# Performance work log

Measured on AMD Instinct MI355X. Metric: run time of the kernel, lower is better.

Reference implementation:

```python
import jax, jax.numpy as jnp
import numpy as np

N_NODES = 100000
N_EDGES = 3200000
D_FEAT = 256
FILTERS = 256


def setup_inputs() -> dict:
    key = jax.random.key(0)
    k1, k2, k3, k4, k5 = jax.random.split(key, 5)
    x = jax.random.normal(k1, (N_NODES, D_FEAT), dtype=jnp.float32)
    edge_row = jax.random.randint(k2, (N_EDGES,), 0, N_NODES, dtype=jnp.int32)
    edge_col = jax.random.randint(k3, (N_EDGES,), 0, N_NODES, dtype=jnp.int32)
    edge_vals = jnp.ones((N_EDGES,), dtype=jnp.float32)
    w = jax.random.normal(k4, (D_FEAT, FILTERS), dtype=jnp.float32) * (2.0 / D_FEAT) ** 0.5  # he_normal
    b = jax.random.normal(k5, (FILTERS,), dtype=jnp.float32) * 0.05
    return {"x": x, "edge_row": edge_row, "edge_col": edge_col,
            "edge_vals": edge_vals, "w": w, "b": b}


def reference(x, edge_row, edge_col, edge_vals, w, b):
    n = x.shape[0]
    # normalize_A: D = rowsum(A); L = D^{-1/2} A D^{-1/2}
    deg = jax.ops.segment_sum(edge_vals, edge_row, num_segments=n)
    dinv = jnp.where(deg > 0, deg ** -0.5, 0.0)  # [N]
    norm_vals = edge_vals * dinv[edge_row] * dinv[edge_col]  # [E]
    # dense projection then sparse aggregation + bias + relu
    h = x @ w  # [N, F]
    msg = norm_vals[:, None] * h[edge_col]  # [E, F] gather + scale
    agg = jax.ops.segment_sum(msg, edge_row, num_segments=n)  # [N, F]
    return jax.nn.relu(agg + b)
```

## Files before the change

### kernel.cpp

```cpp
#include <hip/hip_runtime.h>
#include <hip/hip_bf16.h>


#define DF   256
#define RSH  7
#define RPB  128
#define CAP  4800
#define CHUNK 8192

typedef __attribute__((ext_vector_type(8))) short short8;
typedef __attribute__((ext_vector_type(4))) float f32x4;

__device__ __forceinline__ unsigned short f2bf(float f) {
    unsigned int u = __float_as_uint(f);
    unsigned int r = (u + 0x7fffu + ((u >> 16) & 1u)) >> 16;
    return (unsigned short)r;
}
__device__ __forceinline__ unsigned int pack2(float a, float b) {
    return (unsigned)f2bf(a) | ((unsigned)f2bf(b) << 16);
}
__device__ __forceinline__ float bflo(unsigned int u) { return __uint_as_float(u << 16); }
__device__ __forceinline__ float bfhi(unsigned int u) { return __uint_as_float(u & 0xffff0000u); }

__global__ __launch_bounds__(256) void bhist_kernel(const int* __restrict__ row,
                                                    int* __restrict__ blockhist, int NB, int E) {
    __shared__ int hist[1024];
    int t = threadIdx.x;
    for (int i = t; i < NB; i += 256) hist[i] = 0;
    __syncthreads();
    int base = blockIdx.x * CHUNK;
    int end = base + CHUNK; if (end > E) end = E;
    for (int i = base + t; i < end; i += 256)
        atomicAdd(&hist[row[i] >> RSH], 1);
    __syncthreads();
    for (int i = t; i < NB; i += 256)
        blockhist[(size_t)blockIdx.x * NB + i] = hist[i];
}

__global__ __launch_bounds__(256) void bscan_kernel(int* __restrict__ blockhist,
                                                    int* __restrict__ buckettot, int NB, int NBLK) {
    __shared__ int ps[256];
    int b = blockIdx.x, t = threadIdx.x;
    int e0 = 2 * t, e1 = 2 * t + 1;
    int v0 = (e0 < NBLK) ? blockhist[(size_t)e0 * NB + b] : 0;
    int v1 = (e1 < NBLK) ? blockhist[(size_t)e1 * NB + b] : 0;
    int tsum = v0 + v1;
    ps[t] = tsum;
    __syncthreads();
    for (int off = 1; off < 256; off <<= 1) {
        int v = (t >= off) ? ps[t - off] : 0;
        __syncthreads();
        ps[t] += v;
        __syncthreads();
    }
    int pre = ps[t] - tsum;
    if (e0 < NBLK) blockhist[(size_t)e0 * NB + b] = pre;
    if (e1 < NBLK) blockhist[(size_t)e1 * NB + b] = pre + v0;
    if (t == 255) buckettot[b] = ps[255];
}

__global__ __launch_bounds__(1024) void btot_kernel(const int* __restrict__ buckettot,
                                                    int* __restrict__ bucket_base, int NB) {
    __shared__ int ps[1024];
    int t = threadIdx.x;
    int v = (t < NB) ? buckettot[t] : 0;
    ps[t] = v;
    __syncthreads();
    for (int off = 1; off < 1024; off <<= 1) {
        int u = (t >= off) ? ps[t - off] : 0;
        __syncthreads();
        ps[t] += u;
        __syncthreads();
    }
    if (t < NB) bucket_base[t] = ps[t] - v;
    if (t == 1023) bucket_base[NB] = ps[1023];
}

__global__ __launch_bounds__(256) void bscatter_kernel(const int* __restrict__ row,
                                                       const int* __restrict__ col,
                                                       const float* __restrict__ vals,
                                                       const int* __restrict__ blockhist,
                                                       const int* __restrict__ bucket_base,
                                                       int2* __restrict__ bedge, int NB, int E) {
    __shared__ int loff[1024];
    int t = threadIdx.x, blk = blockIdx.x;
    for (int i = t; i < NB; i += 256)
        loff[i] = bucket_base[i] + blockhist[(size_t)blk * NB + i];
    __syncthreads();
    int base = blk * CHUNK;
    int end = base + CHUNK; if (end > E) end = E;
    for (int i = base + t; i < end; i += 256) {
        int r = row[i];
        int p = atomicAdd(&loff[r >> RSH], 1);
        bedge[p] = make_int2(((r & (RPB - 1)) << 17) | col[i], __float_as_int(vals[i]));
    }
}

__global__ __launch_bounds__(256) void deg_kernel(const int2* __restrict__ bedge,
                                                  const int* __restrict__ bucket_base,
                                                  float* __restrict__ dinv, int N) {
    __shared__ float acc[RPB];
    int b = blockIdx.x, t = threadIdx.x;
    if (t < RPB) acc[t] = 0.f;
    __syncthreads();
    int s = bucket_base[b], e = bucket_base[b + 1];
    for (int i = s + t; i < e; i += 256) {
        int2 ed = bedge[i];
        atomicAdd(&acc[ed.x >> 17], __int_as_float(ed.y));
    }
    __syncthreads();
    if (t < RPB) {
        int r = b * RPB + t;
        if (r < N) {
            float d = acc[t];
            dinv[r] = (d > 0.f) ? (1.0f / sqrtf(d)) : 0.f;
        }
    }
}

__global__ __launch_bounds__(256) void transpose_kernel(const float* __restrict__ w,
                                                        float* __restrict__ wT) {
    __shared__ float tile[32][33];
    int bx = blockIdx.x * 32, by = blockIdx.y * 32;
    int tx = threadIdx.x, ty = threadIdx.y;
    for (int j = ty; j < 32; j += 8) tile[j][tx] = w[(by + j) * DF + bx + tx];
    __syncthreads();
    for (int j = ty; j < 32; j += 8) wT[(bx + j) * DF + by + tx] = tile[tx][j];
}

__global__ __launch_bounds__(256) void gemm_kernel(const float* __restrict__ x,
                                                   const float* __restrict__ wT,
                                                   const float* __restrict__ dinv,
                                                   unsigned short* __restrict__ h, int N) {
    __shared__ unsigned short Al[128 * 32];
    __shared__ unsigned short Bl[128 * 32];
    int tid = threadIdx.x;
    int by = blockIdx.x, bx = blockIdx.y;
    int wv = tid >> 6, lane = tid & 63;
    int wr = wv >> 1, wc = wv & 1;
    int q = lane >> 4, mi = lane & 15;

    f32x4 acc[4][4];
#pragma unroll
    for (int i = 0; i < 4; ++i)
#pragma unroll
        for (int j = 0; j < 4; ++j) acc[i][j] = (f32x4){0.f, 0.f, 0.f, 0.f};

    int srow = tid >> 1;
    int sseg = (tid & 1) * 16;
    int axrow = by * 128 + srow; if (axrow >= N) axrow = N - 1;
    const float* ax = x + (long)axrow * DF + sseg;
    const float* bxp = wT + (long)(bx * 128 + srow) * DF + sseg;
    unsigned short* Aw = &Al[srow * 32 + sseg];
    unsigned short* Bw = &Bl[srow * 32 + sseg];

    for (int kk = 0; kk < DF; kk += 32) {
        float4 a0 = *(const float4*)(ax + kk);
        float4 a1 = *(const float4*)(ax + kk + 4);
        float4 a2 = *(const float4*)(ax + kk + 8);
        float4 a3 = *(const float4*)(ax + kk + 12);
        float4 b0 = *(const float4*)(bxp + kk);
        float4 b1 = *(const float4*)(bxp + kk + 4);
        float4 b2 = *(const float4*)(bxp + kk + 8);
        float4 b3 = *(const float4*)(bxp + kk + 12);
        __syncthreads();
        uint4 pa, pb;
        pa.x = pack2(a0.x, a0.y); pa.y = pack2(a0.z, a0.w);
        pa.z = pack2(a1.x, a1.y); pa.w = pack2(a1.z, a1.w);
        *(uint4*)Aw = pa;
        pa.x = pack2(a2.x, a2.y); pa.y = pack2(a2.z, a2.w);
        pa.z = pack2(a3.x, a3.y); pa.w = pack2(a3.z, a3.w);
        *(uint4*)(Aw + 8) = pa;
        pb.x = pack2(b0.x, b0.y); pb.y = pack2(b0.z, b0.w);
        pb.z = pack2(b1.x, b1.y); pb.w = pack2(b1.z, b1.w);
        *(uint4*)Bw = pb;
        pb.x = pack2(b2.x, b2.y); pb.y = pack2(b2.z, b2.w);
        pb.z = pack2(b3.x, b3.y); pb.w = pack2(b3.z, b3.w);
        *(uint4*)(Bw + 8) = pb;
        __syncthreads();

        short8 af[4], bf[4];
#pragma unroll
        for (int i = 0; i < 4; ++i)
            af[i] = *(const short8*)&Al[(wr * 64 + i * 16 + mi) * 32 + q * 8];
#pragma unroll
        for (int j = 0; j < 4; ++j)
            bf[j] = *(const short8*)&Bl[(wc * 64 + j * 16 + mi) * 32 + q * 8];
#pragma unroll
        for (int i = 0; i < 4; ++i)
#pragma unroll
            for (int j = 0; j < 4; ++j)
                acc[i][j] = __builtin_amdgcn_mfma_f32_16x16x32_bf16(af[i], bf[j], acc[i][j], 0, 0, 0);
    }

#pragma unroll
    for (int i = 0; i < 4; ++i) {
        int base_row = by * 128 + wr * 64 + i * 16 + q * 4;
#pragma unroll
        for (int r = 0; r < 4; ++r) {
            int rg = base_row + r;
            if (rg < N) {
                float dv = dinv[rg];
#pragma unroll
                for (int j = 0; j < 4; ++j) {
                    int cg = bx * 128 + wc * 64 + j * 16 + mi;
                    h[(long)rg * DF + cg] = f2bf(dv * acc[i][j][r]);
                }
            }
        }
    }
}

__global__ __launch_bounds__(256) void aggb_kernel(const unsigned short* __restrict__ h,
                                                   const int2* __restrict__ bedge,
                                                   const int* __restrict__ bucket_base,
                                                   const float* __restrict__ dinv,
                                                   const float* __restrict__ bias,
                                                   float* __restrict__ out, int N) {
    __shared__ int2 ledge[CAP];
    __shared__ int cnt[RPB];
    __shared__ int lrs[RPB + 1];
    __shared__ int lfill[RPB];
    int b = blockIdx.x, t = threadIdx.x;
    int s = bucket_base[b], e = bucket_base[b + 1];
    int tot = e - s;
    int cap_end = s + (tot < CAP ? tot : CAP);
    if (t < RPB) { cnt[t] = 0; lfill[t] = 0; }
    __syncthreads();
    for (int i = s + t; i < cap_end; i += 256)
        atomicAdd(&cnt[bedge[i].x >> 17], 1);
    __syncthreads();
    int myc = 0;
    if (t < RPB) { myc = cnt[t]; lrs[t] = myc; }
    __syncthreads();
    for (int off = 1; off < RPB; off <<= 1) {
        int v = (t < RPB && t >= off) ? lrs[t - off] : 0;
        __syncthreads();
        if (t < RPB) lrs[t] += v;
        __syncthreads();
    }
    if (t < RPB) {
        int iv = lrs[t];
        lrs[t] = iv - myc;
        if (t == RPB - 1) lrs[RPB] = iv;
    }
    __syncthreads();
    for (int i = s + t; i < cap_end; i += 256) {
        int2 ed = bedge[i];
        int rl = ed.x >> 17;
        int p = lrs[rl] + atomicAdd(&lfill[rl], 1);
        ledge[p] = make_int2(ed.x & 0x1FFFF, ed.y);
    }
    __syncthreads();
    int wv = t >> 6, lane = t & 63;
    int half = lane >> 5;
    int fl = (lane & 31) * 8;
    const unsigned short* hp = h + fl;
    for (int lr = wv; lr < RPB; lr += 4) {
        int r = b * RPB + lr;
        if (r >= N) break;
        int rs = lrs[lr], re = lrs[lr + 1];
        float a0 = 0, a1 = 0, a2 = 0, a3 = 0, a4 = 0, a5 = 0, a6 = 0, a7 = 0;
        int i = rs + half;
        for (; i + 6 < re; i += 8) {
            int2 e0 = ledge[i], e1 = ledge[i + 2], e2 = ledge[i + 4], e3 = ledge[i + 6];
            uint4 u0 = *(const uint4*)(hp + (long)e0.x * DF);
            uint4 u1 = *(const uint4*)(hp + (long)e1.x * DF);
            uint4 u2 = *(const uint4*)(hp + (long)e2.x * DF);
            uint4 u3 = *(const uint4*)(hp + (long)e3.x * DF);
            float v0 = __int_as_float(e0.y), v1 = __int_as_float(e1.y);
            float v2 = __int_as_float(e2.y), v3 = __int_as_float(e3.y);
            a0 += v0 * bflo(u0.x) + v1 * bflo(u1.x) + v2 * bflo(u2.x) + v3 * bflo(u3.x);
            a1 += v0 * bfhi(u0.x) + v1 * bfhi(u1.x) + v2 * bfhi(u2.x) + v3 * bfhi(u3.x);
            a2 += v0 * bflo(u0.y) + v1 * bflo(u1.y) + v2 * bflo(u2.y) + v3 * bflo(u3.y);
            a3 += v0 * bfhi(u0.y) + v1 * bfhi(u1.y) + v2 * bfhi(u2.y) + v3 * bfhi(u3.y);
            a4 += v0 * bflo(u0.z) + v1 * bflo(u1.z) + v2 * bflo(u2.z) + v3 * bflo(u3.z);
            a5 += v0 * bfhi(u0.z) + v1 * bfhi(u1.z) + v2 * bfhi(u2.z) + v3 * bfhi(u3.z);
            a6 += v0 * bflo(u0.w) + v1 * bflo(u1.w) + v2 * bflo(u2.w) + v3 * bflo(u3.w);
            a7 += v0 * bfhi(u0.w) + v1 * bfhi(u1.w) + v2 * bfhi(u2.w) + v3 * bfhi(u3.w);
        }
        for (; i < re; i += 2) {
            int2 e0 = ledge[i];
            float v0 = __int_as_float(e0.y);
            uint4 u0 = *(const uint4*)(hp + (long)e0.x * DF);
            a0 += v0 * bflo(u0.x); a1 += v0 * bfhi(u0.x);
            a2 += v0 * bflo(u0.y); a3 += v0 * bfhi(u0.y);
            a4 += v0 * bflo(u0.z); a5 += v0 * bfhi(u0.z);
            a6 += v0 * bflo(u0.w); a7 += v0 * bfhi(u0.w);
        }
        for (int j = cap_end + half; j < e; j += 2) {
            int2 ed = bedge[j];
            if ((ed.x >> 17) == lr) {
                float v0 = __int_as_float(ed.y);
                uint4 u0 = *(const uint4*)(hp + (long)(ed.x & 0x1FFFF) * DF);
                a0 += v0 * bflo(u0.x); a1 += v0 * bfhi(u0.x);
                a2 += v0 * bflo(u0.y); a3 += v0 * bfhi(u0.y);
                a4 += v0 * bflo(u0.z); a5 += v0 * bfhi(u0.z);
                a6 += v0 * bflo(u0.w); a7 += v0 * bfhi(u0.w);
            }
        }
        a0 += __shfl_xor(a0, 32); a1 += __shfl_xor(a1, 32);
        a2 += __shfl_xor(a2, 32); a3 += __shfl_xor(a3, 32);
        a4 += __shfl_xor(a4, 32); a5 += __shfl_xor(a5, 32);
        a6 += __shfl_xor(a6, 32); a7 += __shfl_xor(a7, 32);
        if (half == 0) {
            float dr = dinv[r];
            float4 b0 = *(const float4*)(bias + fl);
            float4 b1 = *(const float4*)(bias + fl + 4);
            float4 o0, o1;
            o0.x = fmaxf(fmaf(dr, a0, b0.x), 0.f);
            o0.y = fmaxf(fmaf(dr, a1, b0.y), 0.f);
            o0.z = fmaxf(fmaf(dr, a2, b0.z), 0.f);
            o0.w = fmaxf(fmaf(dr, a3, b0.w), 0.f);
            o1.x = fmaxf(fmaf(dr, a4, b1.x), 0.f);
            o1.y = fmaxf(fmaf(dr, a5, b1.y), 0.f);
            o1.z = fmaxf(fmaf(dr, a6, b1.z), 0.f);
            o1.w = fmaxf(fmaf(dr, a7, b1.w), 0.f);
            *(float4*)(out + (long)r * DF + fl) = o0;
            *(float4*)(out + (long)r * DF + fl + 4) = o1;
        }
    }
}

extern "C" void kernel_launch(void* const* d_in, const int* in_sizes, int n_in,
                              void* d_out, int out_size, void* d_ws, size_t ws_size,
                              hipStream_t stream) {
    const float* x   = (const float*)d_in[0];
    const int* erow  = (const int*)d_in[1];
    const int* ecol  = (const int*)d_in[2];
    const float* ev  = (const float*)d_in[3];
    const float* w   = (const float*)d_in[4];
    const float* b   = (const float*)d_in[5];
    float* out = (float*)d_out;

    int N = in_sizes[0] / DF;
    int E = in_sizes[1];
    int NB = (N + RPB - 1) >> RSH;
    int NBLK = (E + CHUNK - 1) / CHUNK;

    char* ws = (char*)d_ws;
    size_t Ea8 = (((size_t)E * 8) + 255) & ~(size_t)255;
    size_t Hs  = (((size_t)N * DF * 2) + 255) & ~(size_t)255;
    size_t Na  = (((size_t)N * 4) + 255) & ~(size_t)255;

    int2* bedge = (int2*)ws;
    char* reg2 = ws + Ea8;
    unsigned short* h = (unsigned short*)reg2;
    int* blockhist = (int*)reg2;
    char* reg3 = reg2 + Hs;
    float* wT = (float*)reg3;
    float* dinv = (float*)(reg3 + 262144);
    int* buckettot = (int*)(reg3 + 262144 + Na);
    int* bucket_base = (int*)(reg3 + 262144 + Na + 8192);

    bhist_kernel<<<NBLK, 256, 0, stream>>>(erow, blockhist, NB, E);
    bscan_kernel<<<NB, 256, 0, stream>>>(blockhist, buckettot, NB, NBLK);
    btot_kernel<<<1, 1024, 0, stream>>>(buckettot, bucket_base, NB);
    bscatter_kernel<<<NBLK, 256, 0, stream>>>(erow, ecol, ev, blockhist, bucket_base, bedge, NB, E);
    deg_kernel<<<NB, 256, 0, stream>>>(bedge, bucket_base, dinv, N);
    transpose_kernel<<<dim3(8, 8), dim3(32, 8), 0, stream>>>(w, wT);
    gemm_kernel<<<dim3((N + 127) / 128, DF / 128), 256, 0, stream>>>(x, wT, dinv, h, N);
    aggb_kernel<<<NB, 256, 0, stream>>>(h, bedge, bucket_base, dinv, b, out, N);
}
```

Measured before the change: 595.9 us.

## Build full CSR in degree pass; one-wave-per-row aggregation; full-width bf16 GEMM

The degree kernel now also does the per-bucket counting sort and writes a global CSR (row starts plus sorted col/val pairs). Aggregation then drops the LDS staging, the CAP overflow path and the per-block scans, and runs one wave per row across many small blocks for better occupancy and load balance. The GEMM tiles all 256 output columns per block and reads W already converted to bf16, so x is read and converted only once. The cost is an extra global write and read of the sorted edge array, plus higher accumulator register pressure in the GEMM.

```diff
diff --git a/kernel.cpp b/kernel.cpp
--- a/kernel.cpp
+++ b/kernel.cpp
@@ -5,7 +5,6 @@
 #define DF   256
 #define RSH  7
 #define RPB  128
-#define CAP  4800
 #define CHUNK 8192
 
 typedef __attribute__((ext_vector_type(8))) short short8;
@@ -15,9 +14,6 @@
     unsigned int u = __float_as_uint(f);
     unsigned int r = (u + 0x7fffu + ((u >> 16) & 1u)) >> 16;
     return (unsigned short)r;
-}
-__device__ __forceinline__ unsigned int pack2(float a, float b) {
-    return (unsigned)f2bf(a) | ((unsigned)f2bf(b) << 16);
 }
 __device__ __forceinline__ float bflo(unsigned int u) { return __uint_as_float(u << 16); }
 __device__ __forceinline__ float bfhi(unsigned int u) { return __uint_as_float(u & 0xffff0000u); }
@@ -96,100 +92,128 @@
     }
 }
 
-__global__ __launch_bounds__(256) void deg_kernel(const int2* __restrict__ bedge,
-                                                  const int* __restrict__ bucket_base,
-                                                  float* __restrict__ dinv, int N) {
-    __shared__ float acc[RPB];
+__global__ __launch_bounds__(256) void csrify_kernel(const int2* __restrict__ bedge,
+                                                     const int* __restrict__ bucket_base,
+                                                     int2* __restrict__ scv,
+                                                     int* __restrict__ rstart,
+                                                     float* __restrict__ dinv, int N, int NB) {
+    __shared__ int cnt[RPB];
+    __shared__ float dacc[RPB];
+    __shared__ int lrs[RPB + 1];
+    __shared__ int lfill[RPB];
     int b = blockIdx.x, t = threadIdx.x;
-    if (t < RPB) acc[t] = 0.f;
-    __syncthreads();
     int s = bucket_base[b], e = bucket_base[b + 1];
+    if (t < RPB) { cnt[t] = 0; dacc[t] = 0.f; lfill[t] = 0; }
+    __syncthreads();
     for (int i = s + t; i < e; i += 256) {
         int2 ed = bedge[i];
-        atomicAdd(&acc[ed.x >> 17], __int_as_float(ed.y));
+        int rl = ed.x >> 17;
+        atomicAdd(&cnt[rl], 1);
+        atomicAdd(&dacc[rl], __int_as_float(ed.y));
+    }
+    __syncthreads();
+    int myc = 0;
+    if (t < RPB) { myc = cnt[t]; lrs[t] = myc; }
+    __syncthreads();
+    for (int off = 1; off < RPB; off <<= 1) {
+        int v = (t < RPB && t >= off) ? lrs[t - off] : 0;
+        __syncthreads();
+        if (t < RPB) lrs[t] += v;
+        __syncthreads();
+    }
+    if (t < RPB) {
+        int iv = lrs[t];
+        lrs[t] = iv - myc;
+        if (t == RPB - 1) lrs[RPB] = iv;
     }
     __syncthreads();
     if (t < RPB) {
         int r = b * RPB + t;
         if (r < N) {
-            float d = acc[t];
+            rstart[r] = s + lrs[t];
+            float d = dacc[t];
             dinv[r] = (d > 0.f) ? (1.0f / sqrtf(d)) : 0.f;
         }
     }
+    if (b == NB - 1 && t == 0) rstart[N] = e;
+    for (int i = s + t; i < e; i += 256) {
+        int2 ed = bedge[i];
+        int rl = ed.x >> 17;
+        int p = s + lrs[rl] + atomicAdd(&lfill[rl], 1);
+        scv[p] = make_int2(ed.x & 0x1FFFF, ed.y);
+    }
 }
 
 __global__ __launch_bounds__(256) void transpose_kernel(const float* __restrict__ w,
-                                                        float* __restrict__ wT) {
+                                                        unsigned short* __restrict__ wbf) {
     __shared__ float tile[32][33];
     int bx = blockIdx.x * 32, by = blockIdx.y * 32;
     int tx = threadIdx.x, ty = threadIdx.y;
     for (int j = ty; j < 32; j += 8) tile[j][tx] = w[(by + j) * DF + bx + tx];
     __syncthreads();
-    for (int j = ty; j < 32; j += 8) wT[(bx + j) * DF + by + tx] = tile[tx][j];
+    for (int j = ty; j < 32; j += 8) wbf[(bx + j) * DF + by + tx] = f2bf(tile[tx][j]);
 }
 
 __global__ __launch_bounds__(256) void gemm_kernel(const float* __restrict__ x,
-                                                   const float* __restrict__ wT,
+                                                   const unsigned short* __restrict__ wbf,
                                                    const float* __restrict__ dinv,
                                                    unsigned short* __restrict__ h, int N) {
     __shared__ unsigned short Al[128 * 32];
-    __shared__ unsigned short Bl[128 * 32];
+    __shared__ unsigned short Bl[256 * 32];
     int tid = threadIdx.x;
-    int by = blockIdx.x, bx = blockIdx.y;
+    int by = blockIdx.x;
     int wv = tid >> 6, lane = tid & 63;
     int wr = wv >> 1, wc = wv & 1;
     int q = lane >> 4, mi = lane & 15;
 
-    f32x4 acc[4][4];
+    f32x4 acc[4][8];
 #pragma unroll
     for (int i = 0; i < 4; ++i)
 #pragma unroll
-        for (int j = 0; j < 4; ++j) acc[i][j] = (f32x4){0.f, 0.f, 0.f, 0.f};
+        for (int j = 0; j < 8; ++j) acc[i][j] = (f32x4){0.f, 0.f, 0.f, 0.f};
 
     int srow = tid >> 1;
     int sseg = (tid & 1) * 16;
     int axrow = by * 128 + srow; if (axrow >= N) axrow = N - 1;
     const float* ax = x + (long)axrow * DF + sseg;
-    const float* bxp = wT + (long)(bx * 128 + srow) * DF + sseg;
+    const unsigned short* bx = wbf + (long)tid * DF;
     unsigned short* Aw = &Al[srow * 32 + sseg];
-    unsigned short* Bw = &Bl[srow * 32 + sseg];
+    unsigned short* Bw = &Bl[tid * 32];
 
     for (int kk = 0; kk < DF; kk += 32) {
         float4 a0 = *(const float4*)(ax + kk);
         float4 a1 = *(const float4*)(ax + kk + 4);
         float4 a2 = *(const float4*)(ax + kk + 8);
         float4 a3 = *(const float4*)(ax + kk + 12);
-        float4 b0 = *(const float4*)(bxp + kk);
-        float4 b1 = *(const float4*)(bxp + kk + 4);
-        float4 b2 = *(const float4*)(bxp + kk + 8);
-        float4 b3 = *(const float4*)(bxp + kk + 12);
-        __syncthreads();
-        uint4 pa, pb;
-        pa.x = pack2(a0.x, a0.y); pa.y = pack2(a0.z, a0.w);
-        pa.z = pack2(a1.x, a1.y); pa.w = pack2(a1.z, a1.w);
+        const uint4* wp = (const uint4*)(bx + kk);
+        uint4 b0 = wp[0], b1 = wp[1], b2 = wp[2], b3 = wp[3];
+        __syncthreads();
+        uint4 pa;
+        pa.x = (unsigned)f2bf(a0.x) | ((unsigned)f2bf(a0.y) << 16);
+        pa.y = (unsigned)f2bf(a0.z) | ((unsigned)f2bf(a0.w) << 16);
+        pa.z = (unsigned)f2bf(a1.x) | ((unsigned)f2bf(a1.y) << 16);
+        pa.w = (unsigned)f2bf(a1.z) | ((unsigned)f2bf(a1.w) << 16);
         *(uint4*)Aw = pa;
-        pa.x = pack2(a2.x, a2.y); pa.y = pack2(a2.z, a2.w);
-        pa.z = pack2(a3.x, a3.y); pa.w = pack2(a3.z, a3.w);
+        pa.x = (unsigned)f2bf(a2.x) | ((unsigned)f2bf(a2.y) << 16);
+        pa.y = (unsigned)f2bf(a2.z) | ((unsigned)f2bf(a2.w) << 16);
+        pa.z = (unsigned)f2bf(a3.x) | ((unsigned)f2bf(a3.y) << 16);
+        pa.w = (unsigned)f2bf(a3.z) | ((unsigned)f2bf(a3.w) << 16);
         *(uint4*)(Aw + 8) = pa;
-        pb.x = pack2(b0.x, b0.y); pb.y = pack2(b0.z, b0.w);
-        pb.z = pack2(b1.x, b1.y); pb.w = pack2(b1.z, b1.w);
-        *(uint4*)Bw = pb;
-        pb.x = pack2(b2.x, b2.y); pb.y = pack2(b2.z, b2.w);
-        pb.z = pack2(b3.x, b3.y); pb.w = pack2(b3.z, b3.w);
-        *(uint4*)(Bw + 8) = pb;
-        __syncthreads();
-
-        short8 af[4], bf[4];
+        uint4* bw = (uint4*)Bw;
+        bw[0] = b0; bw[1] = b1; bw[2] = b2; bw[3] = b3;
+        __syncthreads();
+
+        short8 af[4], bf[8];
 #pragma unroll
         for (int i = 0; i < 4; ++i)
             af[i] = *(const short8*)&Al[(wr * 64 + i * 16 + mi) * 32 + q * 8];
 #pragma unroll
-        for (int j = 0; j < 4; ++j)
-            bf[j] = *(const short8*)&Bl[(wc * 64 + j * 16 + mi) * 32 + q * 8];
+        for (int j = 0; j < 8; ++j)
+            bf[j] = *(const short8*)&Bl[(wc * 128 + j * 16 + mi) * 32 + q * 8];
 #pragma unroll
         for (int i = 0; i < 4; ++i)
 #pragma unroll
-            for (int j = 0; j < 4; ++j)
+            for (int j = 0; j < 8; ++j)
                 acc[i][j] = __builtin_amdgcn_mfma_f32_16x16x32_bf16(af[i], bf[j], acc[i][j], 0, 0, 0);
     }
 
@@ -202,8 +226,8 @@
             if (rg < N) {
                 float dv = dinv[rg];
 #pragma unroll
-                for (int j = 0; j < 4; ++j) {
-                    int cg = bx * 128 + wc * 64 + j * 16 + mi;
+                for (int j = 0; j < 8; ++j) {
+                    int cg = wc * 128 + j * 16 + mi;
                     h[(long)rg * DF + cg] = f2bf(dv * acc[i][j][r]);
                 }
             }
@@ -211,114 +235,67 @@
     }
 }
 
-__global__ __launch_bounds__(256) void aggb_kernel(const unsigned short* __restrict__ h,
-                                                   const int2* __restrict__ bedge,
-                                                   const int* __restrict__ bucket_base,
-                                                   const float* __restrict__ dinv,
-                                                   const float* __restrict__ bias,
-                                                   float* __restrict__ out, int N) {
-    __shared__ int2 ledge[CAP];
-    __shared__ int cnt[RPB];
-    __shared__ int lrs[RPB + 1];
-    __shared__ int lfill[RPB];
-    int b = blockIdx.x, t = threadIdx.x;
-    int s = bucket_base[b], e = bucket_base[b + 1];
-    int tot = e - s;
-    int cap_end = s + (tot < CAP ? tot : CAP);
-    if (t < RPB) { cnt[t] = 0; lfill[t] = 0; }
-    __syncthreads();
-    for (int i = s + t; i < cap_end; i += 256)
-        atomicAdd(&cnt[bedge[i].x >> 17], 1);
-    __syncthreads();
-    int myc = 0;
-    if (t < RPB) { myc = cnt[t]; lrs[t] = myc; }
-    __syncthreads();
-    for (int off = 1; off < RPB; off <<= 1) {
-        int v = (t < RPB && t >= off) ? lrs[t - off] : 0;
-        __syncthreads();
-        if (t < RPB) lrs[t] += v;
-        __syncthreads();
-    }
-    if (t < RPB) {
-        int iv = lrs[t];
-        lrs[t] = iv - myc;
-        if (t == RPB - 1) lrs[RPB] = iv;
-    }
-    __syncthreads();
-    for (int i = s + t; i < cap_end; i += 256) {
-        int2 ed = bedge[i];
-        int rl = ed.x >> 17;
-        int p = lrs[rl] + atomicAdd(&lfill[rl], 1);
-        ledge[p] = make_int2(ed.x & 0x1FFFF, ed.y);
-    }
-    __syncthreads();
-    int wv = t >> 6, lane = t & 63;
+__global__ __launch_bounds__(256) void agg_kernel(const unsigned short* __restrict__ h,
+                                                  const int* __restrict__ row_start,
+                                                  const int2* __restrict__ scv,
+                                                  const float* __restrict__ dinv,
+                                                  const float* __restrict__ bias,
+                                                  float* __restrict__ out, int N) {
+    int wave = threadIdx.x >> 6;
+    int lane = threadIdx.x & 63;
+    int r = blockIdx.x * 4 + wave;
+    if (r >= N) return;
     int half = lane >> 5;
     int fl = (lane & 31) * 8;
+    int s = row_start[r], e = row_start[r + 1];
+    float a0 = 0, a1 = 0, a2 = 0, a3 = 0, a4 = 0, a5 = 0, a6 = 0, a7 = 0;
     const unsigned short* hp = h + fl;
-    for (int lr = wv; lr < RPB; lr += 4) {
-        int r = b * RPB + lr;
-        if (r >= N) break;
-        int rs = lrs[lr], re = lrs[lr + 1];
-        float a0 = 0, a1 = 0, a2 = 0, a3 = 0, a4 = 0, a5 = 0, a6 = 0, a7 = 0;
-        int i = rs + half;
-        for (; i + 6 < re; i += 8) {
-            int2 e0 = ledge[i], e1 = ledge[i + 2], e2 = ledge[i + 4], e3 = ledge[i + 6];
-            uint4 u0 = *(const uint4*)(hp + (long)e0.x * DF);
-            uint4 u1 = *(const uint4*)(hp + (long)e1.x * DF);
-            uint4 u2 = *(const uint4*)(hp + (long)e2.x * DF);
-            uint4 u3 = *(const uint4*)(hp + (long)e3.x * DF);
-            float v0 = __int_as_float(e0.y), v1 = __int_as_float(e1.y);
-            float v2 = __int_as_float(e2.y), v3 = __int_as_float(e3.y);
-            a0 += v0 * bflo(u0.x) + v1 * bflo(u1.x) + v2 * bflo(u2.x) + v3 * bflo(u3.x);
-            a1 += v0 * bfhi(u0.x) + v1 * bfhi(u1.x) + v2 * bfhi(u2.x) + v3 * bfhi(u3.x);
-            a2 += v0 * bflo(u0.y) + v1 * bflo(u1.y) + v2 * bflo(u2.y) + v3 * bflo(u3.y);
-            a3 += v0 * bfhi(u0.y) + v1 * bfhi(u1.y) + v2 * bfhi(u2.y) + v3 * bfhi(u3.y);
-            a4 += v0 * bflo(u0.z) + v1 * bflo(u1.z) + v2 * bflo(u2.z) + v3 * bflo(u3.z);
-            a5 += v0 * bfhi(u0.z) + v1 * bfhi(u1.z) + v2 * bfhi(u2.z) + v3 * bfhi(u3.z);
-            a6 += v0 * bflo(u0.w) + v1 * bflo(u1.w) + v2 * bflo(u2.w) + v3 * bflo(u3.w);
-            a7 += v0 * bfhi(u0.w) + v1 * bfhi(u1.w) + v2 * bfhi(u2.w) + v3 * bfhi(u3.w);
-        }
-        for (; i < re; i += 2) {
-            int2 e0 = ledge[i];
-            float v0 = __int_as_float(e0.y);
-            uint4 u0 = *(const uint4*)(hp + (long)e0.x * DF);
-            a0 += v0 * bflo(u0.x); a1 += v0 * bfhi(u0.x);
-            a2 += v0 * bflo(u0.y); a3 += v0 * bfhi(u0.y);
-            a4 += v0 * bflo(u0.z); a5 += v0 * bfhi(u0.z);
-            a6 += v0 * bflo(u0.w); a7 += v0 * bfhi(u0.w);
-        }
-        for (int j = cap_end + half; j < e; j += 2) {
-            int2 ed = bedge[j];
-            if ((ed.x >> 17) == lr) {
-                float v0 = __int_as_float(ed.y);
-                uint4 u0 = *(const uint4*)(hp + (long)(ed.x & 0x1FFFF) * DF);
-                a0 += v0 * bflo(u0.x); a1 += v0 * bfhi(u0.x);
-                a2 += v0 * bflo(u0.y); a3 += v0 * bfhi(u0.y);
-                a4 += v0 * bflo(u0.z); a5 += v0 * bfhi(u0.z);
-                a6 += v0 * bflo(u0.w); a7 += v0 * bfhi(u0.w);
-            }
-        }
-        a0 += __shfl_xor(a0, 32); a1 += __shfl_xor(a1, 32);
-        a2 += __shfl_xor(a2, 32); a3 += __shfl_xor(a3, 32);
-        a4 += __shfl_xor(a4, 32); a5 += __shfl_xor(a5, 32);
-        a6 += __shfl_xor(a6, 32); a7 += __shfl_xor(a7, 32);
-        if (half == 0) {
-            float dr = dinv[r];
-            float4 b0 = *(const float4*)(bias + fl);
-            float4 b1 = *(const float4*)(bias + fl + 4);
-            float4 o0, o1;
-            o0.x = fmaxf(fmaf(dr, a0, b0.x), 0.f);
-            o0.y = fmaxf(fmaf(dr, a1, b0.y), 0.f);
-            o0.z = fmaxf(fmaf(dr, a2, b0.z), 0.f);
-            o0.w = fmaxf(fmaf(dr, a3, b0.w), 0.f);
-            o1.x = fmaxf(fmaf(dr, a4, b1.x), 0.f);
-            o1.y = fmaxf(fmaf(dr, a5, b1.y), 0.f);
-            o1.z = fmaxf(fmaf(dr, a6, b1.z), 0.f);
-            o1.w = fmaxf(fmaf(dr, a7, b1.w), 0.f);
-            *(float4*)(out + (long)r * DF + fl) = o0;
-            *(float4*)(out + (long)r * DF + fl + 4) = o1;
-        }
+    int i = s + half;
+    for (; i + 6 < e; i += 8) {
+        int2 e0 = scv[i], e1 = scv[i + 2], e2 = scv[i + 4], e3 = scv[i + 6];
+        uint4 u0 = *(const uint4*)(hp + (long)e0.x * DF);
+        uint4 u1 = *(const uint4*)(hp + (long)e1.x * DF);
+        uint4 u2 = *(const uint4*)(hp + (long)e2.x * DF);
+        uint4 u3 = *(const uint4*)(hp + (long)e3.x * DF);
+        float v0 = __int_as_float(e0.y), v1 = __int_as_float(e1.y);
+        float v2 = __int_as_float(e2.y), v3 = __int_as_float(e3.y);
+        a0 += v0 * bflo(u0.x) + v1 * bflo(u1.x) + v2 * bflo(u2.x) + v3 * bflo(u3.x);
+        a1 += v0 * bfhi(u0.x) + v1 * bfhi(u1.x) + v2 * bfhi(u2.x) + v3 * bfhi(u3.x);
+        a2 += v0 * bflo(u0.y) + v1 * bflo(u1.y) + v2 * bflo(u2.y) + v3 * bflo(u3.y);
+        a3 += v0 * bfhi(u0.y) + v1 * bfhi(u1.y) + v2 * bfhi(u2.y) + v3 * bfhi(u3.y);
+        a4 += v0 * bflo(u0.z) + v1 * bflo(u1.z) + v2 * bflo(u2.z) + v3 * bflo(u3.z);
+        a5 += v0 * bfhi(u0.z) + v1 * bfhi(u1.z) + v2 * bfhi(u2.z) + v3 * bfhi(u3.z);
+        a6 += v0 * bflo(u0.w) + v1 * bflo(u1.w) + v2 * bflo(u2.w) + v3 * bflo(u3.w);
+        a7 += v0 * bfhi(u0.w) + v1 * bfhi(u1.w) + v2 * bfhi(u2.w) + v3 * bfhi(u3.w);
+    }
+    for (; i < e; i += 2) {
+        int2 e0 = scv[i];
+        float v0 = __int_as_float(e0.y);
+        uint4 u0 = *(const uint4*)(hp + (long)e0.x * DF);
+        a0 += v0 * bflo(u0.x); a1 += v0 * bfhi(u0.x);
+        a2 += v0 * bflo(u0.y); a3 += v0 * bfhi(u0.y);
+        a4 += v0 * bflo(u0.z); a5 += v0 * bfhi(u0.z);
+        a6 += v0 * bflo(u0.w); a7 += v0 * bfhi(u0.w);
+    }
+    a0 += __shfl_xor(a0, 32); a1 += __shfl_xor(a1, 32);
+    a2 += __shfl_xor(a2, 32); a3 += __shfl_xor(a3, 32);
+    a4 += __shfl_xor(a4, 32); a5 += __shfl_xor(a5, 32);
+    a6 += __shfl_xor(a6, 32); a7 += __shfl_xor(a7, 32);
+    if (half == 0) {
+        float dr = dinv[r];
+        float4 b0 = *(const float4*)(bias + fl);
+        float4 b1 = *(const float4*)(bias + fl + 4);
+        float4 o0, o1;
+        o0.x = fmaxf(fmaf(dr, a0, b0.x), 0.f);
+        o0.y = fmaxf(fmaf(dr, a1, b0.y), 0.f);
+        o0.z = fmaxf(fmaf(dr, a2, b0.z), 0.f);
+        o0.w = fmaxf(fmaf(dr, a3, b0.w), 0.f);
+        o1.x = fmaxf(fmaf(dr, a4, b1.x), 0.f);
+        o1.y = fmaxf(fmaf(dr, a5, b1.y), 0.f);
+        o1.z = fmaxf(fmaf(dr, a6, b1.z), 0.f);
+        o1.w = fmaxf(fmaf(dr, a7, b1.w), 0.f);
+        *(float4*)(out + (long)r * DF + fl) = o0;
+        *(float4*)(out + (long)r * DF + fl + 4) = o1;
     }
 }
 
@@ -342,23 +319,26 @@
     size_t Ea8 = (((size_t)E * 8) + 255) & ~(size_t)255;
     size_t Hs  = (((size_t)N * DF * 2) + 255) & ~(size_t)255;
     size_t Na  = (((size_t)N * 4) + 255) & ~(size_t)255;
-
-    int2* bedge = (int2*)ws;
-    char* reg2 = ws + Ea8;
-    unsigned short* h = (unsigned short*)reg2;
-    int* blockhist = (int*)reg2;
-    char* reg3 = reg2 + Hs;
-    float* wT = (float*)reg3;
-    float* dinv = (float*)(reg3 + 262144);
-    int* buckettot = (int*)(reg3 + 262144 + Na);
-    int* bucket_base = (int*)(reg3 + 262144 + Na + 8192);
+    size_t RSa = (((size_t)(N + 1) * 4) + 255) & ~(size_t)255;
+
+    int2* scv = (int2*)ws;
+    char* r2 = ws + Ea8;
+    unsigned short* h = (unsigned short*)r2;
+    int2* bedge = (int2*)r2;
+    int* blockhist = (int*)(r2 + Ea8);
+    char* r3 = r2 + Hs;
+    unsigned short* wbf = (unsigned short*)r3;
+    float* dinv = (float*)(r3 + 131072);
+    int* rstart = (int*)(r3 + 131072 + Na);
+    int* buckettot = (int*)(r3 + 131072 + Na + RSa);
+    int* bucket_base = (int*)(r3 + 131072 + Na + RSa + 4096);
 
     bhist_kernel<<<NBLK, 256, 0, stream>>>(erow, blockhist, NB, E);
     bscan_kernel<<<NB, 256, 0, stream>>>(blockhist, buckettot, NB, NBLK);
     btot_kernel<<<1, 1024, 0, stream>>>(buckettot, bucket_base, NB);
     bscatter_kernel<<<NBLK, 256, 0, stream>>>(erow, ecol, ev, blockhist, bucket_base, bedge, NB, E);
-    deg_kernel<<<NB, 256, 0, stream>>>(bedge, bucket_base, dinv, N);
-    transpose_kernel<<<dim3(8, 8), dim3(32, 8), 0, stream>>>(w, wT);
-    gemm_kernel<<<dim3((N + 127) / 128, DF / 128), 256, 0, stream>>>(x, wT, dinv, h, N);
-    aggb_kernel<<<NB, 256, 0, stream>>>(h, bedge, bucket_base, dinv, b, out, N);
-}
+    csrify_kernel<<<NB, 256, 0, stream>>>(bedge, bucket_base, scv, rstart, dinv, N, NB);
+    transpose_kernel<<<dim3(8, 8), dim3(32, 8), 0, stream>>>(w, wbf);
+    gemm_kernel<<<(N + 127) / 128, 256, 0, stream>>>(x, wbf, dinv, h, N);
+    agg_kernel<<<(N + 3) / 4, 256, 0, stream>>>(h, rstart, scv, dinv, b, out, N);
+}
```

Measured after the change: 616.4 us. 3.4% more time.
